# Optimization experiments

Measured on AMD Instinct MI355X. Metric: run time of the kernel, lower is better.

The kernel has to match this reference:

```python
import jax, jax.numpy as jnp
import numpy as np

ALPHA = -300.0        # softmax sharpness (negative -> weight nearest bin)
IS_QUAN_ON = 1.0      # 1.0 = fully quantized output
B, L, K = 4096, 512, 32


def setup_inputs() -> dict:
    key = jax.random.key(0)
    kx, kb = jax.random.split(key)
    x = jax.random.normal(kx, (B, L, 1), dtype=jnp.float32)
    # codebook bins: sorted scalar centers (kmeans-like init)
    bins = jnp.sort(jax.random.normal(kb, (K,), dtype=jnp.float32))
    return {"x": x, "bins": bins}


def reference(x, bins):
    # x: (B, L, 1), bins: (K,)
    dist = jnp.abs(x - bins.reshape(1, 1, -1))          # (B, L, K)
    soft_assignment = jax.nn.softmax(ALPHA * dist, axis=-1)  # (B, L, K)
    # soft-quantized code: weighted sum of bin values -> (B, L, 1)
    bit_code = jnp.einsum('blk,k->bl', soft_assignment, bins)[..., None]
    bit_code = (1.0 - IS_QUAN_ON) * x + IS_QUAN_ON * bit_code
    return soft_assignment, bit_code
```

## Files before the change

### kernel.cpp

```cpp
#include <hip/hip_runtime.h>


#define SSQ_SCALE (-432.80854f)
#define SSQ_UNROLL 8

typedef float f32x4 __attribute__((ext_vector_type(4)));

template <int CTRL>
__device__ __forceinline__ float dpp_f(float v) {
    int i = __builtin_bit_cast(int, v);
    i = __builtin_amdgcn_update_dpp(i, i, CTRL, 0xf, 0xf, true);
    return __builtin_bit_cast(float, i);
}
#define DPP_XOR1  0xB1
#define DPP_XOR2  0x4E
#define DPP_HMIRR 0x141

__device__ __forceinline__ float red8_min(float v) {
    v = fminf(v, dpp_f<DPP_XOR1>(v));
    v = fminf(v, dpp_f<DPP_XOR2>(v));
    v = fminf(v, dpp_f<DPP_HMIRR>(v));
    return v;
}
__device__ __forceinline__ float red8_sum(float v) {
    v += dpp_f<DPP_XOR1>(v);
    v += dpp_f<DPP_XOR2>(v);
    v += dpp_f<DPP_HMIRR>(v);
    return v;
}

__global__ __launch_bounds__(256) void ssq_kernel(
    const float* __restrict__ x,
    const float* __restrict__ bins,
    float* __restrict__ soft,
    float* __restrict__ code)
{
    const int sub = threadIdx.x & 7;
    const f32x4 b4 = reinterpret_cast<const f32x4*>(bins)[sub];
    f32x4* __restrict__ soft4 = reinterpret_cast<f32x4*>(soft);

    const int base = blockIdx.x * (256 * SSQ_UNROLL) + threadIdx.x;

    float xv[SSQ_UNROLL];
    #pragma unroll
    for (int u = 0; u < SSQ_UNROLL; ++u)
        xv[u] = x[(base + u * 256) >> 3];

    #pragma unroll
    for (int u = 0; u < SSQ_UNROLL; ++u) {
        const int f = base + u * 256;
        const float xu = xv[u];

        const float t0 = xu - b4.x;
        const float t1 = xu - b4.y;
        const float t2 = xu - b4.z;
        const float t3 = xu - b4.w;

        const float dmin = red8_min(
            fminf(fminf(fabsf(t0), fabsf(t1)), fminf(fabsf(t2), fabsf(t3))));

        const float moff = -SSQ_SCALE * dmin;
        const float e0 = __builtin_amdgcn_exp2f(fmaf(SSQ_SCALE, fabsf(t0), moff));
        const float e1 = __builtin_amdgcn_exp2f(fmaf(SSQ_SCALE, fabsf(t1), moff));
        const float e2 = __builtin_amdgcn_exp2f(fmaf(SSQ_SCALE, fabsf(t2), moff));
        const float e3 = __builtin_amdgcn_exp2f(fmaf(SSQ_SCALE, fabsf(t3), moff));

        const float sum = red8_sum((e0 + e1) + (e2 + e3));
        const float num = red8_sum((e0 * b4.x + e1 * b4.y) +
                                   (e2 * b4.z + e3 * b4.w));

        const float inv = __builtin_amdgcn_rcpf(sum);
        f32x4 w;
        w.x = e0 * inv; w.y = e1 * inv; w.z = e2 * inv; w.w = e3 * inv;
        soft4[f] = w;

        if (sub == 0) code[f >> 3] = num * inv;
    }
}

extern "C" void kernel_launch(void* const* d_in, const int* in_sizes, int n_in,
                              void* d_out, int out_size, void* d_ws, size_t ws_size,
                              hipStream_t stream) {
    const float* x    = (const float*)d_in[0];
    const float* bins = (const float*)d_in[1];
    const int n = in_sizes[0];

    float* soft = (float*)d_out;
    float* code = soft + (size_t)n * 32;

    const int total_vec = n * 8;
    const int grid = total_vec / (256 * SSQ_UNROLL);
    ssq_kernel<<<grid, 256, 0, stream>>>(x, bins, soft, code);
}
```

Measured before the change: 57.11 us.

## Process each element with 4 lanes of 8 bins instead of 8 lanes of 4

Changes the thread-to-work mapping so each element's 32 bins are split across 4 lanes holding 8 bins each, not 8 lanes holding 4. This drops one DPP step from each min and sum reduction and makes each lane write two adjacent float4 values. The unroll factor falls from 8 to 2 and the grid is recomputed to match. Fewer cross-lane ops and less per-element overhead are traded for a changed store pattern and less memory-level parallelism per thread.

Result: slower. 61.20 us (+7.1%).

```diff
diff --git a/kernel.cpp b/kernel.cpp
--- a/kernel.cpp
+++ b/kernel.cpp
@@ -2,7 +2,7 @@
 
 
 #define SSQ_SCALE (-432.80854f)
-#define SSQ_UNROLL 8
+#define SSQ_UNROLL 2
 
 typedef float f32x4 __attribute__((ext_vector_type(4)));
 
@@ -14,18 +14,15 @@
 }
 #define DPP_XOR1  0xB1
 #define DPP_XOR2  0x4E
-#define DPP_HMIRR 0x141
 
-__device__ __forceinline__ float red8_min(float v) {
+__device__ __forceinline__ float red4_min(float v) {
     v = fminf(v, dpp_f<DPP_XOR1>(v));
     v = fminf(v, dpp_f<DPP_XOR2>(v));
-    v = fminf(v, dpp_f<DPP_HMIRR>(v));
     return v;
 }
-__device__ __forceinline__ float red8_sum(float v) {
+__device__ __forceinline__ float red4_sum(float v) {
     v += dpp_f<DPP_XOR1>(v);
     v += dpp_f<DPP_XOR2>(v);
-    v += dpp_f<DPP_HMIRR>(v);
     return v;
 }
 
@@ -35,46 +32,60 @@
     float* __restrict__ soft,
     float* __restrict__ code)
 {
-    const int sub = threadIdx.x & 7;
-    const f32x4 b4 = reinterpret_cast<const f32x4*>(bins)[sub];
+    const int sub = threadIdx.x & 3;
+    const f32x4 bA = reinterpret_cast<const f32x4*>(bins)[sub * 2];
+    const f32x4 bB = reinterpret_cast<const f32x4*>(bins)[sub * 2 + 1];
     f32x4* __restrict__ soft4 = reinterpret_cast<f32x4*>(soft);
 
-    const int base = blockIdx.x * (256 * SSQ_UNROLL) + threadIdx.x;
+    const int e0 = blockIdx.x * (64 * SSQ_UNROLL) + (threadIdx.x >> 2);
 
     float xv[SSQ_UNROLL];
     #pragma unroll
     for (int u = 0; u < SSQ_UNROLL; ++u)
-        xv[u] = x[(base + u * 256) >> 3];
+        xv[u] = x[e0 + u * 64];
 
     #pragma unroll
     for (int u = 0; u < SSQ_UNROLL; ++u) {
-        const int f = base + u * 256;
+        const int e = e0 + u * 64;
         const float xu = xv[u];
 
-        const float t0 = xu - b4.x;
-        const float t1 = xu - b4.y;
-        const float t2 = xu - b4.z;
-        const float t3 = xu - b4.w;
+        const float t0 = xu - bA.x, t1 = xu - bA.y;
+        const float t2 = xu - bA.z, t3 = xu - bA.w;
+        const float t4 = xu - bB.x, t5 = xu - bB.y;
+        const float t6 = xu - bB.z, t7 = xu - bB.w;
 
-        const float dmin = red8_min(
-            fminf(fminf(fabsf(t0), fabsf(t1)), fminf(fabsf(t2), fabsf(t3))));
+        const float mA = __builtin_fminf(
+            fminf(fminf(fabsf(t0), fabsf(t1)), fminf(fabsf(t2), fabsf(t3))),
+            fminf(fminf(fabsf(t4), fabsf(t5)), fminf(fabsf(t6), fabsf(t7))));
+        const float dmin = red4_min(mA);
 
         const float moff = -SSQ_SCALE * dmin;
-        const float e0 = __builtin_amdgcn_exp2f(fmaf(SSQ_SCALE, fabsf(t0), moff));
-        const float e1 = __builtin_amdgcn_exp2f(fmaf(SSQ_SCALE, fabsf(t1), moff));
-        const float e2 = __builtin_amdgcn_exp2f(fmaf(SSQ_SCALE, fabsf(t2), moff));
-        const float e3 = __builtin_amdgcn_exp2f(fmaf(SSQ_SCALE, fabsf(t3), moff));
+        const float e0v = __builtin_amdgcn_exp2f(fmaf(SSQ_SCALE, fabsf(t0), moff));
+        const float e1v = __builtin_amdgcn_exp2f(fmaf(SSQ_SCALE, fabsf(t1), moff));
+        const float e2v = __builtin_amdgcn_exp2f(fmaf(SSQ_SCALE, fabsf(t2), moff));
+        const float e3v = __builtin_amdgcn_exp2f(fmaf(SSQ_SCALE, fabsf(t3), moff));
+        const float e4v = __builtin_amdgcn_exp2f(fmaf(SSQ_SCALE, fabsf(t4), moff));
+        const float e5v = __builtin_amdgcn_exp2f(fmaf(SSQ_SCALE, fabsf(t5), moff));
+        const float e6v = __builtin_amdgcn_exp2f(fmaf(SSQ_SCALE, fabsf(t6), moff));
+        const float e7v = __builtin_amdgcn_exp2f(fmaf(SSQ_SCALE, fabsf(t7), moff));
 
-        const float sum = red8_sum((e0 + e1) + (e2 + e3));
-        const float num = red8_sum((e0 * b4.x + e1 * b4.y) +
-                                   (e2 * b4.z + e3 * b4.w));
+        const float sum = red4_sum(((e0v + e1v) + (e2v + e3v)) +
+                                   ((e4v + e5v) + (e6v + e7v)));
+        const float num = red4_sum(((e0v * bA.x + e1v * bA.y) +
+                                    (e2v * bA.z + e3v * bA.w)) +
+                                   ((e4v * bB.x + e5v * bB.y) +
+                                    (e6v * bB.z + e7v * bB.w)));
 
         const float inv = __builtin_amdgcn_rcpf(sum);
-        f32x4 w;
-        w.x = e0 * inv; w.y = e1 * inv; w.z = e2 * inv; w.w = e3 * inv;
-        soft4[f] = w;
+        f32x4 w0, w1;
+        w0.x = e0v * inv; w0.y = e1v * inv; w0.z = e2v * inv; w0.w = e3v * inv;
+        w1.x = e4v * inv; w1.y = e5v * inv; w1.z = e6v * inv; w1.w = e7v * inv;
 
-        if (sub == 0) code[f >> 3] = num * inv;
+        const int q = e * 8 + sub * 2;
+        soft4[q]     = w0;
+        soft4[q + 1] = w1;
+
+        if (sub == 0) code[e] = num * inv;
     }
 }
 
@@ -88,7 +99,6 @@
     float* soft = (float*)d_out;
     float* code = soft + (size_t)n * 32;
 
-    const int total_vec = n * 8;
-    const int grid = total_vec / (256 * SSQ_UNROLL);
+    const int grid = n / (64 * SSQ_UNROLL);
     ssq_kernel<<<grid, 256, 0, stream>>>(x, bins, soft, code);
 }
```
